# Kernel tuning notes

Measured on AMD Instinct MI355X. Metric: run time of the kernel, lower is better.

Reference implementation:

```python
import jax, jax.numpy as jnp
import numpy as np

EPS = 1e-5

def _dh_grid(b):
    # Driscoll-Healy beta grid + quadrature weights (includes sin(beta))
    k = np.arange(2 * b)
    beta = np.pi * (2 * k + 1) / (4 * b)
    j = np.arange(b)
    w = (2.0 / b) * np.sin(beta) * (np.sin(np.outer(beta, 2 * j + 1)) / (2 * j + 1)).sum(1)
    return beta, w

def _wigner_stack(L, betas):
    # d^l_{m m'}(beta) for l<L, zero-padded to slots j=m+(L-1) in a [L,nb,2L-1,2L-1] array.
    betas = np.atleast_1d(np.asarray(betas, np.float64))
    nb = betas.shape[0]
    J = 2 * L - 1
    out = np.zeros((L, nb, J, J), np.float64)
    for l in range(L):
        if l == 0:
            d = np.ones((nb, 1, 1))
        else:
            m = np.arange(-l, l + 1)
            c = np.sqrt(l * (l + 1) - m[:-1] * (m[:-1] + 1.0))
            Jp = np.diag(c, -1).astype(complex)  # raising operator in m=-l..l basis
            Jy = (Jp - Jp.T) / 2j
            ev, V = np.linalg.eigh(Jy)
            ph = np.exp(-1j * betas[:, None] * ev[None, :])
            d = np.einsum('mk,bk,nk->bmn', V, ph, V.conj()).real
        s = (L - 1) - l
        out[l, :, s:s + 2 * l + 1, s:s + 2 * l + 1] = d
    return out

def _constants():
    C = {}
    # layer1: S2 conv b 64 -> 20
    beta1, wq1 = _dh_grid(64)
    d1 = _wigner_stack(20, beta1)
    C['s2_ana'] = jnp.asarray((d1[:, :, :, 19] * wq1[None, :, None] * (2 * np.pi / 128)).astype(np.float32))  # [20,128,39]
    C['half1'] = jnp.asarray(_wigner_stack(20, np.pi / 2)[:, 0, :, 19].astype(np.float32))  # [20,39]
    beta_o1, wq2 = _dh_grid(20)
    ls1 = (2 * np.arange(20) + 1.0)
    C['syn1'] = jnp.asarray((_wigner_stack(20, beta_o1) * ls1[:, None, None, None]).astype(np.float32))  # [20,40,39,39]
    # layer2: SO3 conv b 20 -> 10
    d2 = _wigner_stack(10, beta_o1)
    C['ana2'] = jnp.asarray((d2 * wq2[None, :, None, None] * (2 * np.pi / 40) ** 2).astype(np.float32))  # [10,40,19,19]
    C['half2'] = jnp.asarray(_wigner_stack(10, np.pi / 2)[:, 0].astype(np.float32))  # [10,19,19]
    beta_o2, wq3 = _dh_grid(10)
    ls2 = (2 * np.arange(10) + 1.0)
    C['syn2'] = jnp.asarray((_wigner_stack(10, beta_o2) * ls2[:, None, None, None]).astype(np.float32))  # [10,20,19,19]
    # layer3: SO3 conv b 10 -> 7
    C['ana3'] = jnp.asarray((_wigner_stack(7, beta_o2) * wq3[None, :, None, None] * (2 * np.pi / 20) ** 2).astype(np.float32))  # [7,20,13,13]
    C['half3'] = jnp.asarray(_wigner_stack(7, np.pi / 2)[:, 0].astype(np.float32))  # [7,13,13]
    beta_o3, _ = _dh_grid(7)
    ls3 = (2 * np.arange(7) + 1.0)
    C['syn3'] = jnp.asarray((_wigner_stack(7, beta_o3) * ls3[:, None, None, None]).astype(np.float32))  # [7,14,13,13]
    return C

_C = _constants()

def _so3_ifft(Z, L, d_syn):
    # Z: [L, J, J, B, O] spectral (zero padded); output [B, O, 2L(beta), 2L(alpha), 2L(gamma)]
    M = jnp.einsum('lkjn,ljnbo->bokjn', d_syn, Z)
    N = 2 * L
    J = 2 * L - 1
    idx = (np.arange(J) - (L - 1)) % N
    S = jnp.zeros(M.shape[:3] + (N, N), M.dtype).at[..., idx[:, None], idx[None, :]].set(M)
    return jnp.fft.fft2(S, axes=(-2, -1)).real

def _s2_conv(x, w, bias, C):
    # x: [B, F, 2b_in(beta), 2b_in(alpha)] -> [B, O, 2*20, 2*20, 2*20]
    B, F, K, N = x.shape
    L = 20
    J = 2 * L - 1
    m = np.arange(J) - (L - 1)
    xh = jnp.fft.fft(x, axis=-1)[..., m % N]                       # [B,F,K,J]
    Fx = jnp.einsum('lkj,bfkj->ljbf', C['s2_ana'], xh)             # spherical FFT
    P = w.shape[-1]
    alpha = 2 * np.pi * np.arange(P) / P
    e = jnp.asarray(np.exp(-1j * np.outer(m, alpha)).astype(np.complex64))
    scale = 1.0 / np.sqrt(P * F)
    Ky = jnp.einsum('lj,jp,fop->ljfo', C['half1'], e, w * scale)   # kernel RFT on equatorial grid
    Z = jnp.einsum('ljbf,lnfo->ljnbo', Fx, jnp.conj(Ky))           # s2_mm (outer product over m,n)
    return _so3_ifft(Z, L, C['syn1']) + bias[None, :, None, None, None]

def _so3_conv(x, w, bias, Lo, ana, half, syn):
    # x: [B, F, K(beta), N(alpha), N(gamma)] -> [B, O, 2Lo, 2Lo, 2Lo]
    B, F, K, N, _ = x.shape
    J = 2 * Lo - 1
    m = np.arange(J) - (Lo - 1)
    idx = (-m) % N
    xh = jnp.fft.fft2(x, axes=(-2, -1))[..., idx[:, None], idx[None, :]]  # [B,F,K,J,J]
    Fx = jnp.einsum('lkjn,bfkjn->ljnbf', ana, xh)                  # SO3 FFT
    P = w.shape[-1]
    alpha = 2 * np.pi * np.arange(P) / P
    e = jnp.asarray(np.exp(1j * np.outer(m, alpha)).astype(np.complex64))
    scale = 1.0 / np.sqrt(P * F)
    Ky = jnp.einsum('ljn,jp,fop->ljnfo', half, e, w * scale)       # kernel RFT (beta=pi/2, gamma=0 grid)
    Z = jnp.einsum('ljkbf,lnkfo->ljnbo', Fx, jnp.conj(Ky))         # so3_mm: Z_{mn}=sum_k Fx_{mk} conj(Ky_{nk})
    return _so3_ifft(Z, Lo, syn) + bias[None, :, None, None, None]

def _bn(x, gamma, beta):
    axes = (0,) + tuple(range(2, x.ndim))
    mu = x.mean(axes, keepdims=True)
    var = x.var(axes, keepdims=True)
    shp = (1, -1) + (1,) * (x.ndim - 2)
    return (x - mu) * jax.lax.rsqrt(var + EPS) * gamma.reshape(shp) + beta.reshape(shp)

def _forward(x, w1, b1, g1, bt1, w2, b2, g2, bt2, w3, b3, g3, bt3, w_out, b_out):
    x = _s2_conv(x, w1, b1, _C)
    x = jax.nn.relu(_bn(x, g1, bt1))
    x = _so3_conv(x, w2, b2, 10, _C['ana2'], _C['half2'], _C['syn2'])
    x = jax.nn.relu(_bn(x, g2, bt2))
    x = _so3_conv(x, w3, b3, 7, _C['ana3'], _C['half3'], _C['syn3'])
    x = jax.nn.relu(_bn(x, g3, bt3))
    x = x.reshape(x.shape[0], x.shape[1], -1).max(-1)              # global max pool over SO3 grid
    mu = x.mean(0, keepdims=True)
    var = x.var(0, keepdims=True)
    x = (x - mu) * jax.lax.rsqrt(var + EPS)                        # BatchNorm1d(affine=False)
    x = x @ w_out + b_out
    return jax.nn.log_softmax(x, axis=1)

def setup_inputs():
    key = jax.random.key(0)
    ks = jax.random.split(key, 6)
    B = 16
    return {
        'x': jax.random.normal(ks[0], (B, 6, 128, 128), jnp.float32),
        'w1': jax.random.normal(ks[1], (6, 20, 128), jnp.float32),
        'b1': jnp.zeros((20,), jnp.float32),
        'g1': jnp.ones((20,), jnp.float32),
        'bt1': jnp.zeros((20,), jnp.float32),
        'w2': jax.random.normal(ks[2], (20, 60, 40), jnp.float32),
        'b2': jnp.zeros((60,), jnp.float32),
        'g2': jnp.ones((60,), jnp.float32),
        'bt2': jnp.zeros((60,), jnp.float32),
        'w3': jax.random.normal(ks[3], (60, 100, 20), jnp.float32),
        'b3': jnp.zeros((100,), jnp.float32),
        'g3': jnp.ones((100,), jnp.float32),
        'bt3': jnp.zeros((100,), jnp.float32),
        'w_out': jax.random.normal(ks[4], (100, 55), jnp.float32) * 0.1,
        'b_out': jnp.zeros((55,), jnp.float32),
    }

def reference(x, w1, b1, g1, bt1, w2, b2, g2, bt2, w3, b3, g3, bt3, w_out, b_out):
    return _forward(x, w1, b1, g1, bt1, w2, b2, g2, bt2, w3, b3, g3, bt3, w_out, b_out)
```

## Files before the change

### kernel.cpp

```cpp
#include <hip/hip_runtime.h>
#include <math.h>

#define PI 3.14159265358979323846

__device__ inline int iabs(int x){ return x < 0 ? -x : x; }

__device__ inline void cadd_mul(float2& acc, float2 a, float2 b){
    acc.x += a.x*b.x - a.y*b.y;
    acc.y += a.x*b.y + a.y*b.x;
}
__device__ inline void cadd_mulc(float2& acc, float2 a, float2 b){
    acc.x += a.x*b.x + a.y*b.y;
    acc.y += a.y*b.x - a.x*b.y;
}

__device__ inline double dpowi(double x, int n){
    double r = 1.0;
    for (int i = 0; i < n; ++i) r *= x;
    return r;
}

__device__ double wigner_d(int l, int a, int b, double beta, const double* sf)
{
    double cb = cos(0.5*beta), sb = sin(0.5*beta);
    int smin = max(0, b - a);
    int smax = min(l + b, l - a);
    if (smin > smax) return 0.0;
    double pref = sqrt(sf[l+a]*sf[l-a]*sf[l+b]*sf[l-b]);
    double t = dpowi(cb, 2*l + b - a - 2*smin) * dpowi(sb, a - b + 2*smin);
    if ((a - b + smin) & 1) t = -t;
    double r = -(sb*sb)/(cb*cb);
    double sum = 0.0;
    for (int s = smin; s <= smax; ++s){
        sum += t / (sf[l+b-s]*sf[s]*sf[a-b+s]*sf[l-a-s]);
        t *= r;
    }
    return pref * sum;
}

__global__ void k_wq(double* wq)
{
    int i = blockIdx.x*blockDim.x + threadIdx.x;
    int b, k, off;
    if (i < 128){ b = 64; k = i;      off = 0;   }
    else if (i < 168){ b = 20; k = i-128; off = 128; }
    else if (i < 188){ b = 10; k = i-168; off = 168; }
    else return;
    double beta = PI*(2*k+1)/(4.0*b);
    double s = 0.0;
    for (int j = 0; j < b; ++j) s += sin((2*j+1)*beta)/(2*j+1);
    wq[off+k] = (2.0/b)*sin(beta)*s;
}

__global__ void k_wig_full(float* __restrict__ out, const double* __restrict__ wq,
                           int L, int J, int NB, double denom, double beta_fix,
                           double factor, int mul2l1, int klayout, int jhalf)
{
    __shared__ double sf[40];
    if (threadIdx.x == 0){ sf[0]=1.0; for (int i=1;i<40;i++) sf[i]=sf[i-1]*i; }
    __syncthreads();
    int c0 = (J-1)/2;
    int JROWS = jhalf ? (J+1)/2 : J;
    int idx = blockIdx.x*blockDim.x + threadIdx.x;
    int total = L*NB*JROWS*J;
    if (idx >= total) return;
    int n = idx % J;
    int jj = (idx/J) % JROWS;
    int j = jhalf ? (c0 + jj) : jj;
    int k = (idx/(J*JROWS)) % NB;
    int l = idx/(J*JROWS*NB);
    int mj = j - c0, mn = n - c0;
    float v = 0.f;
    if (iabs(mj) <= l && iabs(mn) <= l){
        double beta = (denom > 0.0) ? PI*(2*k+1)/denom : beta_fix;
        double d = wigner_d(l, mj, mn, beta, sf);
        double mlt = factor * (mul2l1 ? (2.0*l + 1.0) : 1.0);
        if (wq) mlt *= wq[k];
        v = (float)(d*mlt);
    }
    size_t oidx = klayout ? ((size_t)(k*L + l)*J + j)*J + n
                          : ((size_t)(l*NB + k)*J + j)*J + n;
    out[oidx] = v;
}

__global__ void k_wig_col(float* __restrict__ out, const double* __restrict__ wq,
                          int L, int J, int NB, double denom, double beta_fix, double factor,
                          int jhalf)
{
    __shared__ double sf[40];
    if (threadIdx.x == 0){ sf[0]=1.0; for (int i=1;i<40;i++) sf[i]=sf[i-1]*i; }
    __syncthreads();
    int c0 = (J-1)/2;
    int JROWS = jhalf ? (J+1)/2 : J;
    int idx = blockIdx.x*blockDim.x + threadIdx.x;
    int total = L*NB*JROWS;
    if (idx >= total) return;
    int jj = idx % JROWS;
    int j = jhalf ? (c0 + jj) : jj;
    int k = (idx/JROWS) % NB;
    int l = idx/(JROWS*NB);
    int mj = j - c0;
    float v = 0.f;
    if (iabs(mj) <= l){
        double beta = (denom > 0.0) ? PI*(2*k+1)/denom : beta_fix;
        double d = wigner_d(l, mj, 0, beta, sf);
        double mlt = factor;
        if (wq) mlt *= wq[k];
        v = (float)(d*mlt);
    }
    out[(size_t)(l*NB + k)*J + j] = v;
}

__global__ void k_expmat(float2* __restrict__ out, int R, int C, int r0, int c0, int N, double sgn)
{
    int i = blockIdx.x*blockDim.x + threadIdx.x;
    if (i >= R*C) return;
    int c = i % C, r = i / C;
    double ang = sgn*2.0*PI * (double)((r - r0)*(c - c0)) / (double)N;
    out[i] = make_float2((float)cos(ang), (float)sin(ang));
}

__global__ __launch_bounds__(256) void k_dft1(const float* __restrict__ x,
    const float2* __restrict__ E1, float2* __restrict__ xh)
{
    __shared__ float2 sE[4992];
    __shared__ float rows[2048];
    int r0 = blockIdx.x * 16;
    int tid = threadIdx.x;
    for (int i = tid; i < 4992; i += 256) sE[i] = E1[i];
    for (int i = tid; i < 2048; i += 256) rows[i] = x[(size_t)r0*128 + i];
    __syncthreads();
    for (int i = tid; i < 320; i += 256){
        int jj = i % 20, kl = i / 20;
        int j = jj + 19;
        const float* row = &rows[kl*128];
        float2 acc = make_float2(0.f, 0.f);
        for (int a = 0; a < 128; ++a){
            float v = row[a];
            float2 e = sE[a*39 + j];
            acc.x += v*e.x; acc.y += v*e.y;
        }
        xh[(size_t)(r0 + kl)*39 + j] = acc;
    }
}

__global__ void k_fx1(const float* __restrict__ ana, const float2* __restrict__ xh,
                      float2* __restrict__ Fx)
{
    int i = blockIdx.x*blockDim.x + threadIdx.x;
    if (i >= 400) return;
    int hj = i % 20, l = i / 20;
    int j = hj + 19;
    int bf = blockIdx.y;
    const float*  ar = ana + (size_t)l*4992 + j;
    const float2* xr = xh + (size_t)bf*4992 + j;
    float2 acc = make_float2(0.f, 0.f);
    for (int k = 0; k < 128; ++k){
        float a = ar[k*39];
        float2 v = xr[k*39];
        acc.x += a*v.x; acc.y += a*v.y;
    }
    Fx[(size_t)(l*39 + j)*96 + bf] = acc;
}

__global__ void k_wh(float2* __restrict__ wh, const float* __restrict__ w,
                     int J, int P, int F, int O, double sgn)
{
    __shared__ float2 tw[128];
    int tid = threadIdx.x;
    if (tid < P){
        double a = sgn*2.0*PI*tid/P;
        tw[tid] = make_float2((float)cos(a), (float)sin(a));
    }
    __syncthreads();
    int idx = blockIdx.x*blockDim.x + tid;
    if (idx >= J*F*O) return;
    int o = idx % O;
    int f = (idx/O) % F;
    int j = idx/(O*F);
    int mj = j - (J-1)/2;
    int step = ((mj % P) + P) % P;
    const float* wr = w + (f*O+o)*P;
    float2 acc = make_float2(0.f, 0.f);
    int t = 0;
    for (int p = 0; p < P; ++p){
        float v = wr[p];
        acc.x += v*tw[t].x; acc.y += v*tw[t].y;
        t += step; if (t >= P) t -= P;
    }
    wh[idx] = acc;
}

__global__ void k_z1(const float2* __restrict__ Fx, const float2* __restrict__ wh,
                     const float* __restrict__ half1, float2* __restrict__ Z1c, int b0)
{
    int i = blockIdx.x*blockDim.x + threadIdx.x;
    if (i >= 15600) return;
    int bo = blockIdx.y;
    int n = i % 39;
    int lh = i / 39;
    int hj = lh % 20, l = lh / 20;
    int j = hj + 19;
    int b = b0 + bo/20, o = bo % 20;
    float h = half1[l*39 + n] * (1.f/sqrtf(128.f*6.f));
    const float2* fx = Fx + (size_t)(l*39 + j)*96 + b*6;
    const float2* wv = wh + (size_t)n*120 + o;
    float2 acc = make_float2(0.f, 0.f);
    for (int f = 0; f < 6; ++f) cadd_mulc(acc, fx[f], wv[(size_t)f*20]);
    Z1c[(size_t)bo*15600 + i] = make_float2(acc.x*h, acc.y*h);
}

template<int L, int J, int K, int KB, int N, int O, int BS>
__global__ __launch_bounds__(BS) void k_idft_t(const float2* __restrict__ Z,
    const float* __restrict__ syn, const float2* __restrict__ W,
    const float* __restrict__ bias, float* __restrict__ out)
{
    constexpr int JJ = J*J, NN = N*N, c0 = (J-1)/2;
    constexpr int JH = (J+1)/2;
    constexpr int JHJ = JH*J;
    constexpr int LHJ = L*JHJ;
    constexpr int KG = K/KB;
    constexpr int SLOTS = (JHJ + BS - 1)/BS;
    __shared__ float2 sM[KB*JHJ];
    __shared__ float2 sT[JH*N];
    __shared__ float2 sW[J*N];
    int bid = blockIdx.x;
    int kg = bid % KG;
    int bo = bid / KG;
    int k0 = kg*KB;
    int tid = threadIdx.x;

    for (int i = tid; i < J*N; i += BS) sW[i] = W[i];

    float2 acc[SLOTS][KB];
    #pragma unroll
    for (int s = 0; s < SLOTS; ++s)
        #pragma unroll
        for (int kb = 0; kb < KB; ++kb) acc[s][kb] = make_float2(0.f, 0.f);
    #pragma unroll
    for (int s = 0; s < SLOTS; ++s){
        int i = tid + s*BS;
        if (i < JHJ){
            int n = i % J, hj = i / J;
            int lmin = max(hj, iabs(n-c0));
            const float2* zrow = Z + (size_t)bo*LHJ + i;
            const float*  sbase = syn + (size_t)c0*J + i;
            for (int l = lmin; l < L; ++l){
                float2 z = zrow[(size_t)l*JHJ];
                #pragma unroll
                for (int kb = 0; kb < KB; ++kb){
                    float s_ = sbase[(size_t)((k0+kb)*L + l)*JJ];
                    acc[s][kb].x += s_*z.x; acc[s][kb].y += s_*z.y;
                }
            }
        }
    }
    #pragma unroll
    for (int s = 0; s < SLOTS; ++s){
        int i = tid + s*BS;
        if (i < JHJ){
            #pragma unroll
            for (int kb = 0; kb < KB; ++kb) sM[kb*JHJ + i] = acc[s][kb];
        }
    }
    __syncthreads();

    constexpr int RT = (JH+1)/2, CT = N/2;
    for (int kb = 0; kb < KB; ++kb){
        const float2* sMk = &sM[kb*JHJ];
        for (int t = tid; t < RT*CT; t += BS){
            int tg = t % CT, tj = t / CT;
            int h0 = tj*2, g0 = tg*2;
            int h1 = (h0+1 < JH) ? h0+1 : h0;
            float2 a00 = make_float2(0.f,0.f), a01 = make_float2(0.f,0.f);
            float2 a10 = make_float2(0.f,0.f), a11 = make_float2(0.f,0.f);
            for (int n = 0; n < J; ++n){
                float2 w0 = sW[n*N+g0], w1 = sW[n*N+g0+1];
                float2 m0 = sMk[h0*J+n], m1 = sMk[h1*J+n];
                cadd_mul(a00, m0, w0); cadd_mul(a01, m0, w1);
                cadd_mul(a10, m1, w0); cadd_mul(a11, m1, w1);
            }
            sT[h0*N+g0] = a00; sT[h0*N+g0+1] = a01;
            if (h0+1 < JH){ sT[(h0+1)*N+g0] = a10; sT[(h0+1)*N+g0+1] = a11; }
        }
        __syncthreads();
        float bb = bias[bo % O];
        float* obase = out + ((size_t)bo*K + k0 + kb)*NN;
        for (int t = tid; t < CT*CT; t += BS){
            int tg = t % CT, ta = t / CT;
            int a0 = ta*2, g0 = tg*2;
            float2 t00 = sT[g0], t01 = sT[g0+1];
            float r00 = t00.x, r01 = t01.x, r10 = t00.x, r11 = t01.x;
            for (int hj = 1; hj < JH; ++hj){
                float2 wa0 = sW[(c0+hj)*N+a0], wa1 = sW[(c0+hj)*N+a0+1];
                float2 t0 = sT[hj*N+g0], t1 = sT[hj*N+g0+1];
                r00 += 2.f*(t0.x*wa0.x - t0.y*wa0.y);
                r01 += 2.f*(t1.x*wa0.x - t1.y*wa0.y);
                r10 += 2.f*(t0.x*wa1.x - t0.y*wa1.y);
                r11 += 2.f*(t1.x*wa1.x - t1.y*wa1.y);
            }
            obase[(a0+0)*N+g0]   = r00 + bb;
            obase[(a0+0)*N+g0+1] = r01 + bb;
            obase[(a0+1)*N+g0]   = r10 + bb;
            obase[(a0+1)*N+g0+1] = r11 + bb;
        }
        __syncthreads();
    }
}

__global__ __launch_bounds__(256) void k_bn_stats(const float4* __restrict__ x, double* __restrict__ part,
                                                  int B, int C, int S4, int parts)
{
    int c = blockIdx.y, p = blockIdx.x;
    int chunk = (S4 + parts - 1)/parts;
    int s0 = p*chunk, s1e = min(S4, s0 + chunk);
    double a1 = 0.0, a2 = 0.0;
    for (int b = 0; b < B; ++b){
        const float4* base = x + ((size_t)b*C + c)*S4;
        for (int s = s0 + threadIdx.x; s < s1e; s += 256){
            float4 v = base[s];
            a1 += (double)v.x + (double)v.y + (double)v.z + (double)v.w;
            a2 += (double)v.x*v.x + (double)v.y*v.y + (double)v.z*v.z + (double)v.w*v.w;
        }
    }
    __shared__ double r1[256], r2[256];
    r1[threadIdx.x] = a1; r2[threadIdx.x] = a2;
    __syncthreads();
    for (int off = 128; off > 0; off >>= 1){
        if (threadIdx.x < off){ r1[threadIdx.x] += r1[threadIdx.x+off]; r2[threadIdx.x] += r2[threadIdx.x+off]; }
        __syncthreads();
    }
    if (threadIdx.x == 0){ int bid = p*C + c; part[2*bid] = r1[0]; part[2*bid+1] = r2[0]; }
}

__global__ void k_bn_fin(const double* __restrict__ part, const float* __restrict__ g,
                         const float* __restrict__ bt, float2* __restrict__ scsh,
                         int C, int parts, double cnt)
{
    int c = blockIdx.x*blockDim.x + threadIdx.x;
    if (c >= C) return;
    double s1 = 0.0, s2 = 0.0;
    for (int p = 0; p < parts; ++p){ s1 += part[2*(p*C+c)]; s2 += part[2*(p*C+c)+1]; }
    double mu = s1/cnt;
    double var = s2/cnt - mu*mu;
    float sc = (float)(1.0/sqrt(var + 1e-5)) * g[c];
    float sh = bt[c] - (float)mu*sc;
    scsh[c] = make_float2(sc, sh);
}

__global__ __launch_bounds__(256) void k_bn_apply(float4* __restrict__ x, const float2* __restrict__ scsh,
                                                  int C, int S4)
{
    int bc = blockIdx.y;
    float2 p = scsh[bc % C];
    size_t base = (size_t)bc * S4;
    for (int s = blockIdx.x*256 + threadIdx.x; s < S4; s += gridDim.x*256){
        float4 v = x[base + s];
        v.x = fmaxf(fmaf(v.x, p.x, p.y), 0.f);
        v.y = fmaxf(fmaf(v.y, p.x, p.y), 0.f);
        v.z = fmaxf(fmaf(v.z, p.x, p.y), 0.f);
        v.w = fmaxf(fmaf(v.w, p.x, p.y), 0.f);
        x[base + s] = v;
    }
}

template<int N, int J>
__global__ __launch_bounds__(256) void k_dft2_t(const float* __restrict__ x, float2* __restrict__ xh,
                                                const float2* __restrict__ EF)
{
    constexpr int JH = (J+1)/2, c0 = (J-1)/2;
    constexpr int NP = N+1;
    __shared__ float tile[N*NP];
    __shared__ float2 sT[N*J];
    __shared__ float2 sE[N*J];
    int bid = blockIdx.x;
    int tid = threadIdx.x;
    const float* src = x + (size_t)bid*N*N;
    for (int i = tid; i < N*N; i += 256){
        int a = i / N, g = i % N;
        tile[a*NP + g] = src[i];
    }
    for (int i = tid; i < N*J; i += 256) sE[i] = EF[i];
    __syncthreads();
    constexpr int AT = N/2, NT = (J+1)/2;
    for (int t = tid; t < AT*NT; t += 256){
        int tn = t % NT, ta = t / NT;
        int a0 = 2*ta, n0 = 2*tn;
        int n1 = (n0+1 < J) ? n0+1 : n0;
        float2 a00 = make_float2(0.f,0.f), a01 = make_float2(0.f,0.f);
        float2 a10 = make_float2(0.f,0.f), a11 = make_float2(0.f,0.f);
        const float* r0 = &tile[a0*NP];
        const float* r1 = &tile[(a0+1)*NP];
        for (int g = 0; g < N; ++g){
            float v0 = r0[g], v1 = r1[g];
            float2 e0 = sE[g*J+n0], e1 = sE[g*J+n1];
            a00.x += v0*e0.x; a00.y += v0*e0.y;
            a01.x += v0*e1.x; a01.y += v0*e1.y;
            a10.x += v1*e0.x; a10.y += v1*e0.y;
            a11.x += v1*e1.x; a11.y += v1*e1.y;
        }
        sT[a0*J+n0] = a00; sT[(a0+1)*J+n0] = a10;
        if (n0+1 < J){ sT[a0*J+n0+1] = a01; sT[(a0+1)*J+n0+1] = a11; }
    }
    __syncthreads();
    for (int t = tid; t < JH*NT; t += 256){
        int tn = t % NT, hj = t / NT;
        int n0 = 2*tn;
        int n1 = (n0+1 < J) ? n0+1 : n0;
        int j = c0 + hj;
        float2 a0 = make_float2(0.f,0.f), a1 = make_float2(0.f,0.f);
        for (int a = 0; a < N; ++a){
            float2 t0 = sT[a*J+n0], t1 = sT[a*J+n1];
            float2 e = sE[a*J+j];
            cadd_mul(a0, t0, e); cadd_mul(a1, t1, e);
        }
        float2* dst = xh + (size_t)bid*J*J + (size_t)j*J;
        dst[n0] = a0;
        if (n0+1 < J) dst[n0+1] = a1;
    }
}

__global__ void k_fx(const float* __restrict__ ana, const float2* __restrict__ xh,
                     float2* __restrict__ Fx, int L, int J, int JH, int K, int BF)
{
    int i = blockIdx.x*blockDim.x + threadIdx.x;
    int JJ = J*J;
    int total = L*JH*J;
    if (i >= total) return;
    int bf = blockIdx.y;
    int n = i % J;
    int hj = (i / J) % JH;
    int l = i / (J*JH);
    int c0 = (J-1)/2;
    int jn = (c0+hj)*J + n;
    const float*  ar = ana + (size_t)l*K*JJ + jn;
    const float2* xr = xh + (size_t)bf*K*JJ + jn;
    float2 acc = make_float2(0.f, 0.f);
    for (int k = 0; k < K; ++k){
        float a = ar[(size_t)k*JJ];
        float2 v = xr[(size_t)k*JJ];
        acc.x += a*v.x; acc.y += a*v.y;
    }
    Fx[((size_t)l*JJ + jn)*BF + bf] = acc;
}

__global__ void k_h(const float* __restrict__ half, const float2* __restrict__ Fx,
                    float2* __restrict__ H, int L, int J, int JH, int BF)
{
    int idx = blockIdx.x*blockDim.x + threadIdx.x;
    int total = L*JH*J*BF;
    if (idx >= total) return;
    int bf = idx % BF;
    int n = (idx/BF) % J;
    int hj = (idx/(BF*J)) % JH;
    int l = idx/(BF*J*JH);
    int c0 = (J-1)/2;
    int j = c0 + hj;
    const float* hr = half + (l*J+n)*J;
    const float2* fr = Fx + (size_t)(l*J+j)*J*BF + bf;
    float2 acc = make_float2(0.f, 0.f);
    for (int k = 0; k < J; ++k){
        float h = hr[k];
        float2 v = fr[(size_t)k*BF];
        acc.x += h*v.x; acc.y += h*v.y;
    }
    H[((size_t)(l*J+j)*J + n)*BF + bf] = acc;
}

__global__ __launch_bounds__(256) void k_zg(const float2* __restrict__ H,
    const float2* __restrict__ wh, float2* __restrict__ Z,
    int L, int J, int JH, int B, int F, int O, float scale)
{
    extern __shared__ float2 smem[];
    float2* swh = smem;
    float2* sH  = smem + F*O;
    int n = blockIdx.x;
    int b = blockIdx.y;
    int tid = threadIdx.x;
    int c0 = (J-1)/2;
    int LH = L*JH;
    int FO = F*O;
    const float2* whn = wh + (size_t)n*FO;
    for (int i = tid; i < FO; i += 256) swh[i] = whn[i];
    for (int i = tid; i < LH*F; i += 256){
        int f = i % F, lh = i / F;
        int l = lh / JH, hj = lh % JH;
        int lj = l*J + c0 + hj;
        sH[f*LH + lh] = H[((size_t)(lj*J + n)*B + b)*F + f];
    }
    __syncthreads();
    int total = O*LH;
    for (int i = tid; i < total; i += 256){
        int lh = i % LH, o = i / LH;
        float2 acc = make_float2(0.f, 0.f);
        for (int f = 0; f < F; ++f)
            cadd_mulc(acc, sH[f*LH + lh], swh[f*O + o]);
        Z[(size_t)(b*O + o)*LH*J + (size_t)lh*J + n] = make_float2(acc.x*scale, acc.y*scale);
    }
}

__global__ void k_pool(const float* __restrict__ x, float* __restrict__ pooled, int S)
{
    int bid = blockIdx.x;
    const float* base = x + (long long)bid*S;
    float m = -1e30f;
    for (int i = threadIdx.x; i < S; i += blockDim.x) m = fmaxf(m, base[i]);
    __shared__ float r[256];
    r[threadIdx.x] = m;
    __syncthreads();
    for (int off = 128; off > 0; off >>= 1){
        if (threadIdx.x < off) r[threadIdx.x] = fmaxf(r[threadIdx.x], r[threadIdx.x+off]);
        __syncthreads();
    }
    if (threadIdx.x == 0) pooled[bid] = r[0];
}

__global__ __launch_bounds__(256) void k_final(const float* __restrict__ pooled,
    const float* __restrict__ w, const float* __restrict__ bias, float* __restrict__ out)
{
    __shared__ float pn[1600];
    __shared__ float z[880];
    int tid = threadIdx.x;
    for (int f = tid; f < 100; f += 256){
        float s1 = 0.f, s2 = 0.f;
        for (int b = 0; b < 16; ++b){ float v = pooled[b*100+f]; s1 += v; s2 += v*v; }
        float mu = s1/16.f;
        float var = s2/16.f - mu*mu;
        float inv = rsqrtf(var + 1e-5f);
        for (int b = 0; b < 16; ++b) pn[b*100+f] = (pooled[b*100+f]-mu)*inv;
    }
    __syncthreads();
    for (int i = tid; i < 880; i += 256){
        int c = i % 55, b = i/55;
        float acc = bias[c];
        for (int f = 0; f < 100; ++f) acc += pn[b*100+f]*w[f*55+c];
        z[i] = acc;
    }
    __syncthreads();
    for (int b = tid; b < 16; b += 256){
        float m = -1e30f;
        for (int c = 0; c < 55; ++c) m = fmaxf(m, z[b*55+c]);
        float s = 0.f;
        for (int c = 0; c < 55; ++c) s += expf(z[b*55+c]-m);
        float lse = m + logf(s);
        for (int c = 0; c < 55; ++c) out[b*55+c] = z[b*55+c]-lse;
    }
}

static inline int cdiv(long long a, long long b){ return (int)((a + b - 1)/b); }

extern "C" void kernel_launch(void* const* d_in, const int* in_sizes, int n_in,
                              void* d_out, int out_size, void* d_ws, size_t ws_size,
                              hipStream_t stream)
{
    (void)in_sizes; (void)n_in; (void)out_size; (void)ws_size;
    const float* x   = (const float*)d_in[0];
    const float* w1  = (const float*)d_in[1];
    const float* b1  = (const float*)d_in[2];
    const float* g1  = (const float*)d_in[3];
    const float* bt1 = (const float*)d_in[4];
    const float* w2  = (const float*)d_in[5];
    const float* b2  = (const float*)d_in[6];
    const float* g2  = (const float*)d_in[7];
    const float* bt2 = (const float*)d_in[8];
    const float* w3  = (const float*)d_in[9];
    const float* b3  = (const float*)d_in[10];
    const float* g3  = (const float*)d_in[11];
    const float* bt3 = (const float*)d_in[12];
    const float* wo  = (const float*)d_in[13];
    const float* bo  = (const float*)d_in[14];
    float* out = (float*)d_out;
    float* ws  = (float*)d_ws;

    const size_t O_WQ    = 0;
    const size_t O_S2ANA = 376;
    const size_t O_HALF1 = 100216;
    const size_t O_SYN1  = 100996;
    const size_t O_ANA2  = 1317796;
    const size_t O_HALF2 = 1462196;
    const size_t O_SYN2  = 1465806;
    const size_t O_ANA3  = 1538006;
    const size_t O_HALF3 = 1561666;
    const size_t O_SYN3  = 1562849;
    const size_t O_STATS = 1579412;
    const size_t O_PART  = 1580132;
    const size_t O_EF2   = O_PART + 8192;
    const size_t O_EF3   = O_PART + 9712;
    const size_t O_POOL  = 1596516;
    const size_t O_XH1   = 1598116;
    const size_t O_FX1   = 2556580;
    const size_t O_WH1   = 2706340;
    const size_t O_WH2   = 2715700;
    const size_t O_WH3   = 2761300;
    const size_t O_W1    = 2917300;
    const size_t O_W2    = 2920420;
    const size_t O_W3    = 2921180;
    const size_t O_E1    = 2921544;
    const size_t O_A1    = 2931528;
    const size_t O_A2    = 23411528;

    double* WQd   = (double*)(ws + O_WQ);
    float*  S2ANA = ws + O_S2ANA;
    float*  HALF1 = ws + O_HALF1;
    float*  SYN1  = ws + O_SYN1;
    float*  ANA2  = ws + O_ANA2;
    float*  HALF2 = ws + O_HALF2;
    float*  SYN2  = ws + O_SYN2;
    float*  ANA3  = ws + O_ANA3;
    float*  HALF3 = ws + O_HALF3;
    float*  SYN3  = ws + O_SYN3;
    float2* SCSH  = (float2*)(ws + O_STATS);
    double* PART  = (double*)(ws + O_PART);
    float2* EF2   = (float2*)(ws + O_EF2);
    float2* EF3   = (float2*)(ws + O_EF3);
    float*  POOLED= ws + O_POOL;
    float2* XH1   = (float2*)(ws + O_XH1);
    float2* FX1   = (float2*)(ws + O_FX1);
    float2* WH1   = (float2*)(ws + O_WH1);
    float2* WH2   = (float2*)(ws + O_WH2);
    float2* WH3   = (float2*)(ws + O_WH3);
    float2* W1    = (float2*)(ws + O_W1);
    float2* W2    = (float2*)(ws + O_W2);
    float2* W3    = (float2*)(ws + O_W3);
    float2* E1    = (float2*)(ws + O_E1);
    float*  X1    = ws + O_A1;
    float2* FX2   = (float2*)(ws + O_A1);
    float2* H2    = (float2*)(ws + O_A1 + 2310400);
    float2* Z2    = (float2*)(ws + O_A1 + 4620800);
    float2* XH3   = (float2*)(ws + O_A1);
    float2* FX3   = (float2*)(ws + O_A1 + 6489600);
    float2* H3    = (float2*)(ws + O_A1 + 8760960);
    float2* Z3    = (float2*)(ws + O_A1 + 11032320);
    float2* Z1C   = (float2*)(ws + O_A2);
    float2* XH2   = (float2*)(ws + O_A2);
    float*  X2    = ws + O_A2;
    float*  X3    = ws + O_A2;

    const double F128 = 2.0*PI/128.0;
    const double F40sq = (2.0*PI/40.0)*(2.0*PI/40.0);
    const double F20sq = (2.0*PI/20.0)*(2.0*PI/20.0);

    k_wq<<<1, 256, 0, stream>>>(WQd);
    k_wig_col <<<cdiv(20*128*20,256),256,0,stream>>>(S2ANA, WQd,     20, 39, 128, 256.0, 0.0,   F128, 1);
    k_wig_col <<<cdiv(20*39,256),    256,0,stream>>>(HALF1, nullptr, 20, 39, 1,   0.0,   PI/2,  1.0,  0);
    k_wig_full<<<cdiv(624000,256),   256,0,stream>>>(SYN1,  nullptr, 20, 39, 40,  80.0,  0.0,   1.0,   1, 1, 1);
    k_wig_full<<<cdiv(76000,256),    256,0,stream>>>(ANA2,  WQd+128, 10, 19, 40,  80.0,  0.0,   F40sq, 0, 0, 1);
    k_wig_full<<<cdiv(3610,256),     256,0,stream>>>(HALF2, nullptr, 10, 19, 1,   0.0,   PI/2,  1.0,   0, 0, 0);
    k_wig_full<<<cdiv(38000,256),    256,0,stream>>>(SYN2,  nullptr, 10, 19, 20,  40.0,  0.0,   1.0,   1, 1, 1);
    k_wig_full<<<cdiv(12740,256),    256,0,stream>>>(ANA3,  WQd+168, 7,  13, 20,  40.0,  0.0,   F20sq, 0, 0, 1);
    k_wig_full<<<cdiv(1183,256),     256,0,stream>>>(HALF3, nullptr, 7,  13, 1,   0.0,   PI/2,  1.0,   0, 0, 0);
    k_wig_full<<<cdiv(8918,256),     256,0,stream>>>(SYN3,  nullptr, 7,  13, 14,  28.0,  0.0,   1.0,   1, 1, 1);
    k_expmat  <<<cdiv(1560,256),256,0,stream>>>(W1, 39, 40, 19, 0, 40, -1.0);
    k_expmat  <<<cdiv(380,256), 256,0,stream>>>(W2, 19, 20,  9, 0, 20, -1.0);
    k_expmat  <<<cdiv(182,256), 256,0,stream>>>(W3, 13, 14,  6, 0, 14, -1.0);
    k_expmat  <<<cdiv(4992,256),256,0,stream>>>(E1, 128, 39, 0, 19, 128, -1.0);
    k_expmat  <<<cdiv(760,256), 256,0,stream>>>(EF2, 40, 19, 0, 9, 40, +1.0);
    k_expmat  <<<cdiv(260,256), 256,0,stream>>>(EF3, 20, 13, 0, 6, 20, +1.0);

    k_dft1<<<768,256,0,stream>>>(x, E1, XH1);
    k_fx1 <<<dim3(2,96),256,0,stream>>>(S2ANA, XH1, FX1);
    k_wh  <<<cdiv(4680,256),  256,0,stream>>>(WH1, w1, 39, 128, 6, 20, -1.0);
    k_wh  <<<cdiv(22800,256), 256,0,stream>>>(WH2, w2, 19, 40, 20, 60, +1.0);
    k_wh  <<<cdiv(78000,256), 256,0,stream>>>(WH3, w3, 13, 20, 60, 100, +1.0);
    for (int c = 0; c < 2; ++c){
        int b0 = c*8;
        k_z1<<<dim3(cdiv(15600,256),160),256,0,stream>>>(FX1, WH1, HALF1, Z1C, b0);
        k_idft_t<20,39,40,2,40,20,256><<<160*20,256,0,stream>>>(Z1C, SYN1, W1, b1, X1 + (size_t)b0*20*64000);
    }
    k_bn_stats<<<dim3(32,20),256,0,stream>>>((const float4*)X1, PART, 16, 20, 16000, 32);
    k_bn_fin  <<<1,256,0,stream>>>(PART, g1, bt1, SCSH, 20, 32, 16.0*64000.0);
    k_bn_apply<<<dim3(cdiv(16000,256),320),256,0,stream>>>((float4*)X1, SCSH, 20, 16000);

    k_dft2_t<40,19><<<12800,256,0,stream>>>(X1, XH2, EF2);
    k_fx  <<<dim3(cdiv(1900,256),320),256,0,stream>>>(ANA2, XH2, FX2, 10, 19, 10, 40, 320);
    k_h   <<<cdiv(608000,256),256,0,stream>>>(HALF2, FX2, H2, 10, 19, 10, 320);
    k_zg  <<<dim3(19,16),256,(1200+2000)*sizeof(float2),stream>>>(H2, WH2, Z2, 10, 19, 10, 16, 20, 60, 1.f/sqrtf(800.f));
    k_idft_t<10,19,20,5,20,60,256><<<960*4,256,0,stream>>>(Z2, SYN2, W2, b2, X2);
    k_bn_stats<<<dim3(8,60),256,0,stream>>>((const float4*)X2, PART, 16, 60, 2000, 8);
    k_bn_fin  <<<1,256,0,stream>>>(PART, g2, bt2, SCSH+20, 60, 8, 16.0*8000.0);
    k_bn_apply<<<dim3(cdiv(2000,256),960),256,0,stream>>>((float4*)X2, SCSH+20, 60, 2000);

    k_dft2_t<20,13><<<19200,256,0,stream>>>(X2, XH3, EF3);
    k_fx  <<<dim3(cdiv(637,256),960),256,0,stream>>>(ANA3, XH3, FX3, 7, 13, 7, 20, 960);
    k_h   <<<cdiv(611520,256),256,0,stream>>>(HALF3, FX3, H3, 7, 13, 7, 960);
    k_zg  <<<dim3(13,16),256,(6000+2940)*sizeof(float2),stream>>>(H3, WH3, Z3, 7, 13, 7, 16, 60, 100, 1.f/sqrtf(1200.f));
    k_idft_t<7,13,14,7,14,100,256><<<1600*2,256,0,stream>>>(Z3, SYN3, W3, b3, X3);
    k_bn_stats<<<dim3(8,100),256,0,stream>>>((const float4*)X3, PART, 16, 100, 686, 8);
    k_bn_fin  <<<1,256,0,stream>>>(PART, g3, bt3, SCSH+80, 100, 8, 16.0*2744.0);
    k_bn_apply<<<dim3(cdiv(686,256),1600),256,0,stream>>>((float4*)X3, SCSH+80, 100, 686);

    k_pool <<<1600,256,0,stream>>>(X3, POOLED, 2744);
    k_final<<<1,256,0,stream>>>(POOLED, wo, bo, out);
}
```

Baseline: 972.9 us.

## Fuse BN apply+ReLU into downstream DFT and pool kernels; widen DFT register tiles

Removes the three standalone batch-norm apply kernels and instead applies the scale/shift plus ReLU while loading tiles in the DFT kernels and inside the max-pool. This saves a full read-modify-write pass over each activation tensor. The DFT kernel's register tiling also grows from 2 to 4 rows in the first stage and 2x2 in the second. That gives more reuse per load at the cost of more registers per thread.

Result: slower. 1.229 ms (+26.3%).

```diff
diff --git a/kernel.cpp b/kernel.cpp
--- a/kernel.cpp
+++ b/kernel.cpp
@@ -348,25 +348,10 @@
     scsh[c] = make_float2(sc, sh);
 }
 
-__global__ __launch_bounds__(256) void k_bn_apply(float4* __restrict__ x, const float2* __restrict__ scsh,
-                                                  int C, int S4)
-{
-    int bc = blockIdx.y;
-    float2 p = scsh[bc % C];
-    size_t base = (size_t)bc * S4;
-    for (int s = blockIdx.x*256 + threadIdx.x; s < S4; s += gridDim.x*256){
-        float4 v = x[base + s];
-        v.x = fmaxf(fmaf(v.x, p.x, p.y), 0.f);
-        v.y = fmaxf(fmaf(v.y, p.x, p.y), 0.f);
-        v.z = fmaxf(fmaf(v.z, p.x, p.y), 0.f);
-        v.w = fmaxf(fmaf(v.w, p.x, p.y), 0.f);
-        x[base + s] = v;
-    }
-}
-
 template<int N, int J>
 __global__ __launch_bounds__(256) void k_dft2_t(const float* __restrict__ x, float2* __restrict__ xh,
-                                                const float2* __restrict__ EF)
+                                                const float2* __restrict__ EF,
+                                                const float2* __restrict__ scsh, int KBETA, int C)
 {
     constexpr int JH = (J+1)/2, c0 = (J-1)/2;
     constexpr int NP = N+1;
@@ -375,48 +360,66 @@
     __shared__ float2 sE[N*J];
     int bid = blockIdx.x;
     int tid = threadIdx.x;
+    float2 p = scsh[(bid / KBETA) % C];
     const float* src = x + (size_t)bid*N*N;
     for (int i = tid; i < N*N; i += 256){
         int a = i / N, g = i % N;
-        tile[a*NP + g] = src[i];
+        tile[a*NP + g] = fmaxf(fmaf(src[i], p.x, p.y), 0.f);
     }
     for (int i = tid; i < N*J; i += 256) sE[i] = EF[i];
     __syncthreads();
-    constexpr int AT = N/2, NT = (J+1)/2;
+    constexpr int AT = N/4, NT = (J+1)/2;
     for (int t = tid; t < AT*NT; t += 256){
         int tn = t % NT, ta = t / NT;
-        int a0 = 2*ta, n0 = 2*tn;
+        int a0 = 4*ta, n0 = 2*tn;
         int n1 = (n0+1 < J) ? n0+1 : n0;
         float2 a00 = make_float2(0.f,0.f), a01 = make_float2(0.f,0.f);
         float2 a10 = make_float2(0.f,0.f), a11 = make_float2(0.f,0.f);
-        const float* r0 = &tile[a0*NP];
+        float2 a20 = make_float2(0.f,0.f), a21 = make_float2(0.f,0.f);
+        float2 a30 = make_float2(0.f,0.f), a31 = make_float2(0.f,0.f);
+        const float* r0 = &tile[(a0+0)*NP];
         const float* r1 = &tile[(a0+1)*NP];
+        const float* r2 = &tile[(a0+2)*NP];
+        const float* r3 = &tile[(a0+3)*NP];
         for (int g = 0; g < N; ++g){
-            float v0 = r0[g], v1 = r1[g];
+            float v0 = r0[g], v1 = r1[g], v2 = r2[g], v3 = r3[g];
             float2 e0 = sE[g*J+n0], e1 = sE[g*J+n1];
-            a00.x += v0*e0.x; a00.y += v0*e0.y;
-            a01.x += v0*e1.x; a01.y += v0*e1.y;
-            a10.x += v1*e0.x; a10.y += v1*e0.y;
-            a11.x += v1*e1.x; a11.y += v1*e1.y;
-        }
-        sT[a0*J+n0] = a00; sT[(a0+1)*J+n0] = a10;
-        if (n0+1 < J){ sT[a0*J+n0+1] = a01; sT[(a0+1)*J+n0+1] = a11; }
-    }
-    __syncthreads();
-    for (int t = tid; t < JH*NT; t += 256){
-        int tn = t % NT, hj = t / NT;
-        int n0 = 2*tn;
+            a00.x += v0*e0.x; a00.y += v0*e0.y;  a01.x += v0*e1.x; a01.y += v0*e1.y;
+            a10.x += v1*e0.x; a10.y += v1*e0.y;  a11.x += v1*e1.x; a11.y += v1*e1.y;
+            a20.x += v2*e0.x; a20.y += v2*e0.y;  a21.x += v2*e1.x; a21.y += v2*e1.y;
+            a30.x += v3*e0.x; a30.y += v3*e0.y;  a31.x += v3*e1.x; a31.y += v3*e1.y;
+        }
+        sT[(a0+0)*J+n0] = a00; sT[(a0+1)*J+n0] = a10;
+        sT[(a0+2)*J+n0] = a20; sT[(a0+3)*J+n0] = a30;
+        if (n0+1 < J){
+            sT[(a0+0)*J+n0+1] = a01; sT[(a0+1)*J+n0+1] = a11;
+            sT[(a0+2)*J+n0+1] = a21; sT[(a0+3)*J+n0+1] = a31;
+        }
+    }
+    __syncthreads();
+    constexpr int RT2 = (JH+1)/2;
+    for (int t = tid; t < RT2*NT; t += 256){
+        int tn = t % NT, th = t / NT;
+        int h0 = 2*th, n0 = 2*tn;
+        int h1 = (h0+1 < JH) ? h0+1 : h0;
         int n1 = (n0+1 < J) ? n0+1 : n0;
-        int j = c0 + hj;
-        float2 a0 = make_float2(0.f,0.f), a1 = make_float2(0.f,0.f);
+        int j0 = c0 + h0, j1 = c0 + h1;
+        float2 a00 = make_float2(0.f,0.f), a01 = make_float2(0.f,0.f);
+        float2 a10 = make_float2(0.f,0.f), a11 = make_float2(0.f,0.f);
         for (int a = 0; a < N; ++a){
             float2 t0 = sT[a*J+n0], t1 = sT[a*J+n1];
-            float2 e = sE[a*J+j];
-            cadd_mul(a0, t0, e); cadd_mul(a1, t1, e);
-        }
-        float2* dst = xh + (size_t)bid*J*J + (size_t)j*J;
-        dst[n0] = a0;
-        if (n0+1 < J) dst[n0+1] = a1;
+            float2 e0 = sE[a*J+j0], e1 = sE[a*J+j1];
+            cadd_mul(a00, t0, e0); cadd_mul(a01, t1, e0);
+            cadd_mul(a10, t0, e1); cadd_mul(a11, t1, e1);
+        }
+        float2* dst0 = xh + (size_t)bid*J*J + (size_t)j0*J;
+        dst0[n0] = a00;
+        if (n0+1 < J) dst0[n0+1] = a01;
+        if (h0+1 < JH){
+            float2* dst1 = xh + (size_t)bid*J*J + (size_t)j1*J;
+            dst1[n0] = a10;
+            if (n0+1 < J) dst1[n0+1] = a11;
+        }
     }
 }
 
@@ -499,12 +502,15 @@
     }
 }
 
-__global__ void k_pool(const float* __restrict__ x, float* __restrict__ pooled, int S)
+__global__ void k_pool(const float* __restrict__ x, float* __restrict__ pooled, int S,
+                       const float2* __restrict__ scsh, int C)
 {
     int bid = blockIdx.x;
+    float2 p = scsh[bid % C];
     const float* base = x + (long long)bid*S;
-    float m = -1e30f;
-    for (int i = threadIdx.x; i < S; i += blockDim.x) m = fmaxf(m, base[i]);
+    float m = 0.f;
+    for (int i = threadIdx.x; i < S; i += blockDim.x)
+        m = fmaxf(m, fmaf(base[i], p.x, p.y));
     __shared__ float r[256];
     r[threadIdx.x] = m;
     __syncthreads();
@@ -512,7 +518,7 @@
         if (threadIdx.x < off) r[threadIdx.x] = fmaxf(r[threadIdx.x], r[threadIdx.x+off]);
         __syncthreads();
     }
-    if (threadIdx.x == 0) pooled[bid] = r[0];
+    if (threadIdx.x == 0) pooled[bid] = fmaxf(r[0], 0.f);
 }
 
 __global__ __launch_bounds__(256) void k_final(const float* __restrict__ pooled,
@@ -669,26 +675,23 @@
     }
     k_bn_stats<<<dim3(32,20),256,0,stream>>>((const float4*)X1, PART, 16, 20, 16000, 32);
     k_bn_fin  <<<1,256,0,stream>>>(PART, g1, bt1, SCSH, 20, 32, 16.0*64000.0);
-    k_bn_apply<<<dim3(cdiv(16000,256),320),256,0,stream>>>((float4*)X1, SCSH, 20, 16000);
-
-    k_dft2_t<40,19><<<12800,256,0,stream>>>(X1, XH2, EF2);
+
+    k_dft2_t<40,19><<<12800,256,0,stream>>>(X1, XH2, EF2, SCSH, 40, 20);
     k_fx  <<<dim3(cdiv(1900,256),320),256,0,stream>>>(ANA2, XH2, FX2, 10, 19, 10, 40, 320);
     k_h   <<<cdiv(608000,256),256,0,stream>>>(HALF2, FX2, H2, 10, 19, 10, 320);
     k_zg  <<<dim3(19,16),256,(1200+2000)*sizeof(float2),stream>>>(H2, WH2, Z2, 10, 19, 10, 16, 20, 60, 1.f/sqrtf(800.f));
     k_idft_t<10,19,20,5,20,60,256><<<960*4,256,0,stream>>>(Z2, SYN2, W2, b2, X2);
     k_bn_stats<<<dim3(8,60),256,0,stream>>>((const float4*)X2, PART, 16, 60, 2000, 8);
     k_bn_fin  <<<1,256,0,stream>>>(PART, g2, bt2, SCSH+20, 60, 8, 16.0*8000.0);
-    k_bn_apply<<<dim3(cdiv(2000,256),960),256,0,stream>>>((float4*)X2, SCSH+20, 60, 2000);
-
-    k_dft2_t<20,13><<<19200,256,0,stream>>>(X2, XH3, EF3);
+
+    k_dft2_t<20,13><<<19200,256,0,stream>>>(X2, XH3, EF3, SCSH+20, 20, 60);
     k_fx  <<<dim3(cdiv(637,256),960),256,0,stream>>>(ANA3, XH3, FX3, 7, 13, 7, 20, 960);
     k_h   <<<cdiv(611520,256),256,0,stream>>>(HALF3, FX3, H3, 7, 13, 7, 960);
     k_zg  <<<dim3(13,16),256,(6000+2940)*sizeof(float2),stream>>>(H3, WH3, Z3, 7, 13, 7, 16, 60, 100, 1.f/sqrtf(1200.f));
     k_idft_t<7,13,14,7,14,100,256><<<1600*2,256,0,stream>>>(Z3, SYN3, W3, b3, X3);
     k_bn_stats<<<dim3(8,100),256,0,stream>>>((const float4*)X3, PART, 16, 100, 686, 8);
     k_bn_fin  <<<1,256,0,stream>>>(PART, g3, bt3, SCSH+80, 100, 8, 16.0*2744.0);
-    k_bn_apply<<<dim3(cdiv(686,256),1600),256,0,stream>>>((float4*)X3, SCSH+80, 100, 686);
-
-    k_pool <<<1600,256,0,stream>>>(X3, POOLED, 2744);
+
+    k_pool <<<1600,256,0,stream>>>(X3, POOLED, 2744, SCSH+80, 100);
     k_final<<<1,256,0,stream>>>(POOLED, wo, bo, out);
 }
```
